# Kernel optimization log

Hardware: AMD Instinct MI355X
Metric: run time of the kernel (lower is better)

Reference implementation:

```python
import jax, jax.numpy as jnp
import numpy as np

SEQ_LEN, BATCH, INPUT_SIZE, HIDDEN = 512, 64, 256, 512


def setup_inputs() -> dict:
    key = jax.random.key(0)
    k_x, k_wih, k_whh, k_bih, k_bhh = jax.random.split(key, 5)
    bound = 1.0 / np.sqrt(HIDDEN)  # torch nn.RNN init: U(-1/sqrt(H), 1/sqrt(H))
    x = jax.random.normal(k_x, (SEQ_LEN, BATCH, INPUT_SIZE), dtype=jnp.float32)
    h0 = jnp.zeros((1, BATCH, HIDDEN), dtype=jnp.float32)
    W_ih = jax.random.uniform(k_wih, (HIDDEN, INPUT_SIZE), minval=-bound, maxval=bound, dtype=jnp.float32)
    W_hh = jax.random.uniform(k_whh, (HIDDEN, HIDDEN), minval=-bound, maxval=bound, dtype=jnp.float32)
    b_ih = jax.random.uniform(k_bih, (HIDDEN,), minval=-bound, maxval=bound, dtype=jnp.float32)
    b_hh = jax.random.uniform(k_bhh, (HIDDEN,), minval=-bound, maxval=bound, dtype=jnp.float32)
    return {"x": x, "h0": h0, "W_ih": W_ih, "W_hh": W_hh, "b_ih": b_ih, "b_hh": b_hh}


def reference(x, h0, W_ih, W_hh, b_ih, b_hh):
    # Elman RNN: h_t = tanh(W_ih x_t + b_ih + W_hh h_{t-1} + b_hh)
    # Precompute the input projection for all timesteps (one big GEMM),
    # then scan the sequential recurrence.
    xW = jnp.einsum('tbi,hi->tbh', x, W_ih) + b_ih + b_hh  # (T, B, H)

    def step(h, xw_t):
        h_new = jnp.tanh(xw_t + h @ W_hh.T)  # (B, H)
        return h_new, h_new

    h_last, h_seq = jax.lax.scan(step, h0[0], xW)
    return h_seq, h_last[None]  # (T, B, H), (1, B, H)
```

## Files before the change

### kernel.cpp

```cpp
#include <hip/hip_runtime.h>


#define T_LEN 512
#define NBATCH 64
#define ISZ 256
#define HSZ 512

typedef __attribute__((ext_vector_type(8))) short short8;
typedef __attribute__((ext_vector_type(4))) int int4v;
typedef __attribute__((ext_vector_type(4))) float f32x4;

#define LOG2E2f 2.8853900817779268f
#define DEQ2C ((float)(2.8853900817779268 / (127.0 * 127.0 * 22.627416997969522)))

__device__ __forceinline__ unsigned short f2bf(float f) {
  unsigned u = __float_as_uint(f);
  u += 0x7fffu + ((u >> 16) & 1u);
  return (unsigned short)(u >> 16);
}
__device__ __forceinline__ float bf2f(unsigned short h) {
  return __uint_as_float(((unsigned)h) << 16);
}

__device__ __forceinline__ void split_bf(f32x4 a, f32x4 b, short8& hi, short8& lo) {
#pragma unroll
  for (int i = 0; i < 4; ++i) {
    unsigned short h = f2bf(a[i]);
    hi[i] = (short)h;
    lo[i] = (short)f2bf(a[i] - bf2f(h));
    unsigned short h2 = f2bf(b[i]);
    hi[i + 4] = (short)h2;
    lo[i + 4] = (short)f2bf(b[i] - bf2f(h2));
  }
}

__global__ __launch_bounds__(512) void xw_proj(
    const float* __restrict__ x, const float* __restrict__ Wih,
    const float* __restrict__ bih, const float* __restrict__ bhh,
    float* __restrict__ out) {
  __shared__ __align__(16) short xhi[16][264];
  __shared__ __align__(16) short xlo[16][264];

  const int tid = threadIdx.x;
  const int w  = tid >> 6;
  const int L  = tid & 63;
  const int lr = L & 15;
  const int lg = L >> 4;

  const int mhalf = blockIdx.x & 1;
  const int grp   = blockIdx.x >> 1;

  short8 Ahi[2][8], Alo[2][8];
  f32x4 bias[2];
  int mt[2];
#pragma unroll
  for (int m = 0; m < 2; ++m) {
    mt[m] = mhalf * 16 + 2 * w + m;
    int j = mt[m] * 16 + lr;
#pragma unroll
    for (int kt = 0; kt < 8; ++kt) {
      int k = kt * 32 + lg * 8;
      const f32x4 v0 = *(const f32x4*)(Wih + j * ISZ + k);
      const f32x4 v1 = *(const f32x4*)(Wih + j * ISZ + k + 4);
      split_bf(v0, v1, Ahi[m][kt], Alo[m][kt]);
    }
    int j0 = mt[m] * 16 + lg * 4;
    f32x4 b1 = *(const f32x4*)(bih + j0);
    f32x4 b2 = *(const f32x4*)(bhh + j0);
    bias[m] = (b1 + b2) * LOG2E2f;
  }

  for (int it = 0; it < 8; ++it) {
    const int tau = grp * 8 + it;
    const int t = tau >> 2;
    const int g = tau & 3;

    __syncthreads();
    {
      const int f   = tid * 8;
      const int row = f >> 8;
      const int i0  = f & 255;
      const float* p = x + ((size_t)(t * NBATCH + g * 16 + row) * ISZ + i0);
      const f32x4 v0 = *(const f32x4*)p;
      const f32x4 v1 = *(const f32x4*)(p + 4);
      short8 hi, lo;
      split_bf(v0, v1, hi, lo);
      *(short8*)(&xhi[row][i0]) = hi;
      *(short8*)(&xlo[row][i0]) = lo;
    }
    __syncthreads();

    f32x4 acc[2];
    acc[0] = f32x4{0.f, 0.f, 0.f, 0.f};
    acc[1] = f32x4{0.f, 0.f, 0.f, 0.f};
#pragma unroll
    for (int kt = 0; kt < 8; ++kt) {
      int koff = kt * 32 + lg * 8;
      short8 bh = *(const short8*)(&xhi[lr][koff]);
      short8 bl = *(const short8*)(&xlo[lr][koff]);
      acc[0] = __builtin_amdgcn_mfma_f32_16x16x32_bf16(Ahi[0][kt], bh, acc[0], 0, 0, 0);
      acc[1] = __builtin_amdgcn_mfma_f32_16x16x32_bf16(Ahi[1][kt], bh, acc[1], 0, 0, 0);
      acc[0] = __builtin_amdgcn_mfma_f32_16x16x32_bf16(Alo[0][kt], bh, acc[0], 0, 0, 0);
      acc[1] = __builtin_amdgcn_mfma_f32_16x16x32_bf16(Alo[1][kt], bh, acc[1], 0, 0, 0);
      acc[0] = __builtin_amdgcn_mfma_f32_16x16x32_bf16(Ahi[0][kt], bl, acc[0], 0, 0, 0);
      acc[1] = __builtin_amdgcn_mfma_f32_16x16x32_bf16(Ahi[1][kt], bl, acc[1], 0, 0, 0);
    }
#pragma unroll
    for (int m = 0; m < 2; ++m) {
      f32x4 r = acc[m] * LOG2E2f + bias[m];
      *(f32x4*)(out + (size_t)((((t * 4 + g) * 32 + mt[m]) * 64) + L) * 4) = r;
    }
  }
}

__global__ __launch_bounds__(1024, 4) void rnn_scan_i8(
    const float* __restrict__ Whh, const float* __restrict__ h0,
    float* __restrict__ out) {
  __shared__ __align__(16) char hb[2 * 16 * 528];

  const int tid = threadIdx.x;
  const int w  = tid >> 6;
  const int L  = tid & 63;
  const int lr = L & 15;
  const int lg = L >> 4;
  const int g  = blockIdx.x;

  const float QS = 127.0f * 22.627416997969522f;

  int4v A[2][8];
#pragma unroll
  for (int m = 0; m < 2; ++m) {
    const int j = (2 * w + m) * 16 + lr;
#pragma unroll
    for (int kt = 0; kt < 8; ++kt) {
      const float* p = Whh + (size_t)j * HSZ + kt * 64 + lg * 16;
      int dw[4];
#pragma unroll
      for (int d = 0; d < 4; ++d) {
        f32x4 v = *(const f32x4*)(p + d * 4);
        int pk = 0;
#pragma unroll
        for (int i = 0; i < 4; ++i) {
          float q = __builtin_rintf(fminf(fmaxf(v[i] * QS, -127.f), 127.f));
          pk |= ((int)q & 255) << (8 * i);
        }
        dw[d] = pk;
      }
      A[m][kt] = int4v{dw[0], dw[1], dw[2], dw[3]};
    }
  }

  if (tid < 512) {
    const int row = tid >> 5;
    const int k0  = (tid & 31) * 16;
    const float* p = h0 + ((size_t)(g * 16 + row) * HSZ + k0);
    int dw[4];
#pragma unroll
    for (int c = 0; c < 4; ++c) {
      f32x4 v = *(const f32x4*)(p + c * 4);
      int pk = 0;
#pragma unroll
      for (int i = 0; i < 4; ++i) {
        float q = __builtin_rintf(fminf(fmaxf(v[i] * 127.f, -127.f), 127.f));
        pk |= ((int)q & 255) << (8 * i);
      }
      dw[c] = pk;
    }
    *(int4v*)(&hb[row * 528 + k0]) = int4v{dw[0], dw[1], dw[2], dw[3]};
  }
  __syncthreads();

  const int j0 = 32 * w + lg * 4;
  const char* xwp = (const char*)out + ((size_t)(g * 32 + 2 * w) * 64 + L) * 16;
  float* hsp = out + (size_t)(g * 16 + lr) * HSZ + j0;
  const int ldsr = lr * 528 + lg * 16;
  const int ldsw = lr * 528 + j0;

  f32x4 pend[2];
  f32x4 xwA[2], xwB[2];

#pragma unroll
  for (int m = 0; m < 2; ++m) xwA[m] = *(const f32x4*)(xwp + m * 1024);
  xwp += 131072;

#define RNN_STEP(XWC, XWN, P, DOSTORE) do {                                    \
    _Pragma("unroll")                                                          \
    for (int m = 0; m < 2; ++m) XWN[m] = *(const f32x4*)(xwp + m * 1024);      \
    xwp += 131072;                                                             \
    if (DOSTORE) {                                                             \
      _Pragma("unroll")                                                        \
      for (int m = 0; m < 2; ++m) *(f32x4*)(hsp + m * 16) = pend[m];           \
      hsp += NBATCH * HSZ;                                                     \
    }                                                                          \
    int4v B[8];                                                                \
    _Pragma("unroll")                                                          \
    for (int kt = 0; kt < 8; ++kt)                                             \
      B[kt] = *(const int4v*)(&hb[(P) * 8448 + ldsr + kt * 64]);               \
    int4v acc[2];                                                              \
    acc[0] = int4v{0, 0, 0, 0};                                                \
    acc[1] = int4v{0, 0, 0, 0};                                                \
    _Pragma("unroll")                                                          \
    for (int kt = 0; kt < 8; ++kt) {                                           \
      acc[0] = __builtin_amdgcn_mfma_i32_16x16x64_i8(A[0][kt], B[kt],          \
                                                     acc[0], 0, 0, 0);         \
      acc[1] = __builtin_amdgcn_mfma_i32_16x16x64_i8(A[1][kt], B[kt],          \
                                                     acc[1], 0, 0, 0);         \
    }                                                                          \
    _Pragma("unroll")                                                          \
    for (int m = 0; m < 2; ++m) {                                              \
      unsigned qi[4];                                                          \
      f32x4 hh;                                                                \
      _Pragma("unroll")                                                        \
      for (int r = 0; r < 4; ++r) {                                            \
        float y2 = fmaf((float)acc[m][r], DEQ2C, XWC[m][r]);                   \
        float e  = __builtin_amdgcn_exp2f(y2);                     \
        float rc = __builtin_amdgcn_rcpf(1.0f + e);                            \
        float hv = fmaf(-2.0f, rc, 1.0f);                         \
        hh[r] = hv;                                                            \
        qi[r] = __float_as_uint(fmaf(hv, 127.0f, 12582912.0f));                \
      }                                                                        \
      pend[m] = hh;                                                            \
      unsigned pp0 = __builtin_amdgcn_perm(qi[1], qi[0], 0x0c0c0400u);         \
      unsigned pp1 = __builtin_amdgcn_perm(qi[3], qi[2], 0x04000c0cu);         \
      *(unsigned*)(&hb[(1 - (P)) * 8448 + ldsw + m * 16]) = pp0 | pp1;         \
    }                                                                          \
    asm volatile("s_waitcnt lgkmcnt(0)\n\ts_barrier" ::: "memory");            \
  } while (0)

  RNN_STEP(xwA, xwB, 0, 0);
  for (int it = 0; it < 255; ++it) {
    RNN_STEP(xwB, xwA, 1, 1);
    RNN_STEP(xwA, xwB, 0, 1);
  }
  RNN_STEP(xwB, xwA, 1, 1);
#undef RNN_STEP

#pragma unroll
  for (int m = 0; m < 2; ++m) {
    *(f32x4*)(hsp + m * 16) = pend[m];
    *(f32x4*)(out + (size_t)T_LEN * NBATCH * HSZ +
              (size_t)(g * 16 + lr) * HSZ + j0 + m * 16) = pend[m];
  }
}

extern "C" void kernel_launch(void* const* d_in, const int* in_sizes, int n_in,
                              void* d_out, int out_size, void* d_ws, size_t ws_size,
                              hipStream_t stream) {
  const float* x   = (const float*)d_in[0];
  const float* h0  = (const float*)d_in[1];
  const float* Wih = (const float*)d_in[2];
  const float* Whh = (const float*)d_in[3];
  const float* bih = (const float*)d_in[4];
  const float* bhh = (const float*)d_in[5];
  float* out = (float*)d_out;

  xw_proj<<<512, 512, 0, stream>>>(x, Wih, bih, bhh, out);
  rnn_scan_i8<<<4, 1024, 0, stream>>>(Whh, h0, out);
}
```

Before: 933.5 us.

## Interleave LDS reads with MFMAs and rotate K order per wave

```diff
diff --git a/kernel.cpp b/kernel.cpp
--- a/kernel.cpp
+++ b/kernel.cpp
@@ -12,6 +12,8 @@
 
 #define LOG2E2f 2.8853900817779268f
 #define DEQ2C ((float)(2.8853900817779268 / (127.0 * 127.0 * 22.627416997969522)))
+
+#define SGB __builtin_amdgcn_sched_group_barrier
 
 __device__ __forceinline__ unsigned short f2bf(float f) {
   unsigned u = __float_as_uint(f);
@@ -125,6 +127,8 @@
   const int lg = L >> 4;
   const int g  = blockIdx.x;
 
+  const int rot = (w & 3) << 1;
+
   const float QS = 127.0f * 22.627416997969522f;
 
   int4v A[2][8];
@@ -132,7 +136,8 @@
   for (int m = 0; m < 2; ++m) {
     const int j = (2 * w + m) * 16 + lr;
 #pragma unroll
-    for (int kt = 0; kt < 8; ++kt) {
+    for (int jj = 0; jj < 8; ++jj) {
+      const int kt = (rot + jj) & 7;
       const float* p = Whh + (size_t)j * HSZ + kt * 64 + lg * 16;
       int dw[4];
 #pragma unroll
@@ -146,7 +151,7 @@
         }
         dw[d] = pk;
       }
-      A[m][kt] = int4v{dw[0], dw[1], dw[2], dw[3]};
+      A[m][jj] = int4v{dw[0], dw[1], dw[2], dw[3]};
     }
   }
 
@@ -176,12 +181,34 @@
   const int ldsr = lr * 528 + lg * 16;
   const int ldsw = lr * 528 + j0;
 
+  const int ko0 = ((rot + 0) & 7) * 64;
+  const int ko1 = ((rot + 1) & 7) * 64;
+  const int ko2 = ((rot + 2) & 7) * 64;
+  const int ko3 = ((rot + 3) & 7) * 64;
+  const int ko4 = ((rot + 4) & 7) * 64;
+  const int ko5 = ((rot + 5) & 7) * 64;
+  const int ko6 = ((rot + 6) & 7) * 64;
+  const int ko7 = ((rot + 7) & 7) * 64;
+
   f32x4 pend[2];
   f32x4 xwA[2], xwB[2];
 
 #pragma unroll
   for (int m = 0; m < 2; ++m) xwA[m] = *(const f32x4*)(xwp + m * 1024);
   xwp += 131072;
+
+#define SLOT_RD(J, RJ) do {                                                    \
+    B##RJ = *(const int4v*)(&hb[cb_ + ldsr + ko##RJ]);                         \
+    acc0 = __builtin_amdgcn_mfma_i32_16x16x64_i8(A[0][J], B##J, acc0, 0, 0, 0);\
+    acc1 = __builtin_amdgcn_mfma_i32_16x16x64_i8(A[1][J], B##J, acc1, 0, 0, 0);\
+    SGB(0x100, 1, 0);                                           \
+    SGB(0x8, 2, 0);                                             \
+  } while (0)
+#define SLOT_NR(J) do {                                                        \
+    acc0 = __builtin_amdgcn_mfma_i32_16x16x64_i8(A[0][J], B##J, acc0, 0, 0, 0);\
+    acc1 = __builtin_amdgcn_mfma_i32_16x16x64_i8(A[1][J], B##J, acc1, 0, 0, 0);\
+    SGB(0x8, 2, 0);                                             \
+  } while (0)
 
 #define RNN_STEP(XWC, XWN, P, DOSTORE) do {                                    \
     _Pragma("unroll")                                                          \
@@ -192,27 +219,33 @@
       for (int m = 0; m < 2; ++m) *(f32x4*)(hsp + m * 16) = pend[m];           \
       hsp += NBATCH * HSZ;                                                     \
     }                                                                          \
-    int4v B[8];                                                                \
-    _Pragma("unroll")                                                          \
-    for (int kt = 0; kt < 8; ++kt)                                             \
-      B[kt] = *(const int4v*)(&hb[(P) * 8448 + ldsr + kt * 64]);               \
-    int4v acc[2];                                                              \
-    acc[0] = int4v{0, 0, 0, 0};                                                \
-    acc[1] = int4v{0, 0, 0, 0};                                                \
-    _Pragma("unroll")                                                          \
-    for (int kt = 0; kt < 8; ++kt) {                                           \
-      acc[0] = __builtin_amdgcn_mfma_i32_16x16x64_i8(A[0][kt], B[kt],          \
-                                                     acc[0], 0, 0, 0);         \
-      acc[1] = __builtin_amdgcn_mfma_i32_16x16x64_i8(A[1][kt], B[kt],          \
-                                                     acc[1], 0, 0, 0);         \
-    }                                                                          \
+    const int cb_ = (P) * 8448;                                                \
+    int4v B0, B1, B2, B3, B4, B5, B6, B7;                                      \
+                                                     \
+    B0 = *(const int4v*)(&hb[cb_ + ldsr + ko0]);                               \
+    B1 = *(const int4v*)(&hb[cb_ + ldsr + ko1]);                               \
+    B2 = *(const int4v*)(&hb[cb_ + ldsr + ko2]);                               \
+    SGB(0x100, 3, 0);                                                          \
+    int4v acc0 = int4v{0, 0, 0, 0};                                            \
+    int4v acc1 = int4v{0, 0, 0, 0};                                            \
+    __builtin_amdgcn_s_setprio(1);                                             \
+    SLOT_RD(0, 3);                                                             \
+    SLOT_RD(1, 4);                                                             \
+    SLOT_RD(2, 5);                                                             \
+    SLOT_RD(3, 6);                                                             \
+    SLOT_RD(4, 7);                                                             \
+    SLOT_NR(5);                                                                \
+    SLOT_NR(6);                                                                \
+    SLOT_NR(7);                                                                \
+    __builtin_amdgcn_s_setprio(0);                                             \
     _Pragma("unroll")                                                          \
     for (int m = 0; m < 2; ++m) {                                              \
       unsigned qi[4];                                                          \
       f32x4 hh;                                                                \
+      const int4v am = m ? acc1 : acc0;                                        \
       _Pragma("unroll")                                                        \
       for (int r = 0; r < 4; ++r) {                                            \
-        float y2 = fmaf((float)acc[m][r], DEQ2C, XWC[m][r]);                   \
+        float y2 = fmaf((float)am[r], DEQ2C, XWC[m][r]);                       \
         float e  = __builtin_amdgcn_exp2f(y2);                     \
         float rc = __builtin_amdgcn_rcpf(1.0f + e);                            \
         float hv = fmaf(-2.0f, rc, 1.0f);                         \
@@ -234,6 +267,8 @@
   }
   RNN_STEP(xwB, xwA, 1, 1);
 #undef RNN_STEP
+#undef SLOT_RD
+#undef SLOT_NR
 
 #pragma unroll
   for (int m = 0; m < 2; ++m) {
```

Result: faster. 832.9 us (-10.8%).
